# Optimization experiments

Hardware: AMD Instinct MI355X
Metric: run time of the kernel (lower is better)

Reference implementation:

```python
import jax, jax.numpy as jnp
import numpy as np

B, T, H, L, O = 128, 1024, 512, 2, 1
SCALE = 0.02  # keep tanh/sigmoid in sane range


def setup_inputs() -> dict:
    key = jax.random.key(0)
    ks = jax.random.split(key, 13)
    return {
        "input": jax.random.normal(ks[0], (B, 8), jnp.float32),
        "hidden": jax.random.normal(ks[1], (L, B, H), jnp.float32) * 0.5,
        "encoder_outputs": jax.random.normal(ks[2], (B, T, H), jnp.float32),
        "attn_w": jax.random.normal(ks[3], (1, (L + 1) * H), jnp.float32) * SCALE,
        "attn_b": jnp.zeros((1,), jnp.float32),
        "comb_w": jax.random.normal(ks[4], (H, H + O), jnp.float32) * SCALE,
        "comb_b": jnp.zeros((H,), jnp.float32),
        "gru_w_ih": jax.random.normal(ks[5], (L, 3 * H, H), jnp.float32) * SCALE,
        "gru_w_hh": jax.random.normal(ks[6], (L, 3 * H, H), jnp.float32) * SCALE,
        "gru_b_ih": jnp.zeros((L, 3 * H), jnp.float32),
        "gru_b_hh": jnp.zeros((L, 3 * H), jnp.float32),
        "out_w": jax.random.normal(ks[7], (O, H), jnp.float32) * SCALE,
        "out_b": jnp.zeros((O,), jnp.float32),
    }


def reference(input, hidden, encoder_outputs, attn_w, attn_b, comb_w, comb_b,
              gru_w_ih, gru_w_hh, gru_b_ih, gru_b_hh, out_w, out_b):
    # input0 = input[:, -1].unsqueeze(1) -> [B, 1]
    input0 = input[:, -1:]
    # hidden [L,B,H] -> hidden_attn [B, L*H]
    hidden_attn = jnp.transpose(hidden, (1, 0, 2)).reshape(hidden.shape[1], -1)
    # Vectorized additive-attention scores (original loops over T):
    # score[b,t] = [hidden_attn_b ; enc_bt] @ attn_w.T + attn_b
    w = attn_w[0]                      # [(L+1)*H]
    w_h, w_e = w[: L * H], w[L * H:]   # [L*H], [H]
    score = (hidden_attn @ w_h)[:, None] + jnp.einsum('bth,h->bt', encoder_outputs, w_e) + attn_b[0]
    attn_weights = jax.nn.softmax(score, axis=1)          # [B, T]
    attn_applied = jnp.einsum('bt,bth->bh', attn_weights, encoder_outputs)  # [B, H]
    # attn_combine + relu (dropout_p = 0 -> identity)
    comb_in = jnp.concatenate([input0, attn_applied], axis=1)  # [B, 1+H]
    x = jax.nn.relu(comb_in @ comb_w.T + comb_b)               # [B, H]
    # single-step multi-layer GRU (PyTorch gate order: r, z, n)
    new_hidden = []
    for l in range(L):
        gx = x @ gru_w_ih[l].T + gru_b_ih[l]             # [B, 3H]
        gh = hidden[l] @ gru_w_hh[l].T + gru_b_hh[l]     # [B, 3H]
        xr, xz, xn = jnp.split(gx, 3, axis=1)
        hr, hz, hn = jnp.split(gh, 3, axis=1)
        r = jax.nn.sigmoid(xr + hr)
        z = jax.nn.sigmoid(xz + hz)
        n = jnp.tanh(xn + r * hn)
        h_new = (1.0 - z) * n + z * hidden[l]
        new_hidden.append(h_new)
        x = h_new
    hidden_out = jnp.stack(new_hidden, axis=0)           # [L, B, H]
    output = x @ out_w.T + out_b                         # [B, O]
    return output, hidden_out, attn_weights[:, None, :]
```

## Files before the change

### kernel.cpp

```cpp
#include <hip/hip_runtime.h>
#include <math.h>

#define B 128
#define T 1024
#define H 512
#define L 2
#define G3H 1536
#define C 8
#define TC 128
#define TT 8
#define NT (TC / TT)
#define KS 2

#define GLOBAL_AS __attribute__((address_space(1)))
#define LDS_AS    __attribute__((address_space(3)))

typedef __attribute__((ext_vector_type(8))) short bf16x8;
typedef __attribute__((ext_vector_type(4))) float f32x4;

__global__ __launch_bounds__(256, 4)
void attn_fused_kernel(const float* __restrict__ enc,
                       const float* __restrict__ attn_w,
                       float* __restrict__ score_out,
                       float* __restrict__ part,
                       float* __restrict__ stats) {
    int c = blockIdx.x, b = blockIdx.y;
    int tid = threadIdx.x, lane = tid & 63, wave = tid >> 6;
    __shared__ float tile[2][TT * H];
    __shared__ float s_tile[TT];

    const float4 we0 = *(const float4*)(attn_w + L * H + lane * 8);
    const float4 we1 = *(const float4*)(attn_w + L * H + lane * 8 + 4);

    const float* encb = enc + ((size_t)b * T + c * TC) * H;
    const GLOBAL_AS float* gsrc = (const GLOBAL_AS float*)encb;
    LDS_AS float* ldst = (LDS_AS float*)(&tile[0][0]);

#define STAGE(buf, t0)                                                        \
    {                                                                         \
        const GLOBAL_AS float* g = gsrc + (size_t)(t0) * H;                   \
        LDS_AS float* lb = ldst + (buf) * (TT * H);                           \
        _Pragma("unroll")                                                     \
        for (int k = 0; k < 4; k++) {                                         \
            __builtin_amdgcn_global_load_lds(                                 \
                (const GLOBAL_AS void*)(g + k * 1024 + tid * 4),              \
                (LDS_AS void*)(lb + k * 1024 + tid * 4), 16, 0, 0);           \
        }                                                                     \
    }

    float m_run = -1e30f, l_run = 0.0f;
    float accx = 0.0f, accy = 0.0f;

    STAGE(0, 0);
    for (int t = 0; t < NT; t++) {
        __syncthreads();
        if (t + 1 < NT) STAGE((t + 1) & 1, (t + 1) * TT);
        const float* tb = &tile[t & 1][0];

#pragma unroll
        for (int r = 0; r < 2; r++) {
            int row = wave * 2 + r;
            const float* tr = tb + row * H + lane * 8;
            float4 e0 = *(const float4*)(tr);
            float4 e1 = *(const float4*)(tr + 4);
            float d = e0.x * we0.x + e0.y * we0.y + e0.z * we0.z + e0.w * we0.w
                    + e1.x * we1.x + e1.y * we1.y + e1.z * we1.z + e1.w * we1.w;
#pragma unroll
            for (int off = 32; off; off >>= 1) d += __shfl_xor(d, off);
            if (lane == 0) {
                s_tile[row] = d;
                score_out[b * T + c * TC + t * TT + row] = d;
            }
        }
        __builtin_amdgcn_s_waitcnt(0xC07F);
        __builtin_amdgcn_s_barrier();

        float sarr[TT], tmax = -1e30f;
#pragma unroll
        for (int i = 0; i < TT; i++) {
            sarr[i] = s_tile[i];
            tmax = fmaxf(tmax, sarr[i]);
        }
        float m_new = fmaxf(m_run, tmax);
        float alpha = __expf(m_run - m_new);
        accx *= alpha; accy *= alpha;
        float wsum = 0.0f;
#pragma unroll
        for (int i = 0; i < TT; i++) {
            float w = __expf(sarr[i] - m_new);
            wsum += w;
            accx += w * tb[i * H + tid];
            accy += w * tb[i * H + tid + 256];
        }
        l_run = l_run * alpha + wsum;
        m_run = m_new;
    }
    part[((size_t)c * B + b) * H + tid]       = accx;
    part[((size_t)c * B + b) * H + tid + 256] = accy;
    if (tid == 0) {
        stats[(c * B + b) * 2]     = m_run;
        stats[(c * B + b) * 2 + 1] = l_run;
    }
#undef STAGE
}

__global__ void comb_kernel(const float* __restrict__ part,
                            const float* __restrict__ stats,
                            const float* __restrict__ score,
                            const float* __restrict__ input,
                            const float* __restrict__ comb_w,
                            const float* __restrict__ comb_b,
                            float* __restrict__ x_out,
                            float* __restrict__ attnw) {
    int q = blockIdx.x, b = blockIdx.y, tid = threadIdx.x;
    int lane = tid & 63, wave = tid >> 6;
    __shared__ float at[H];

    float mc[C], lc[C], m_fin = -1e30f;
#pragma unroll
    for (int k = 0; k < C; k++) {
        mc[k] = stats[(k * B + b) * 2];
        lc[k] = stats[(k * B + b) * 2 + 1];
        m_fin = fmaxf(m_fin, mc[k]);
    }
    float l_fin = 0.0f;
#pragma unroll
    for (int k = 0; k < C; k++) l_fin += lc[k] * __expf(mc[k] - m_fin);
    float inv = 1.0f / l_fin;
    float ax = 0.0f, ay = 0.0f;
#pragma unroll
    for (int k = 0; k < C; k++) {
        float sc = __expf(mc[k] - m_fin);
        ax += sc * part[((size_t)k * B + b) * H + tid];
        ay += sc * part[((size_t)k * B + b) * H + tid + 256];
    }
    at[tid]       = ax * inv;
    at[tid + 256] = ay * inv;
    if (q == 0) {
        float4 sv = *(const float4*)(score + b * T + tid * 4);
        float4 ov = { __expf(sv.x - m_fin) * inv, __expf(sv.y - m_fin) * inv,
                      __expf(sv.z - m_fin) * inv, __expf(sv.w - m_fin) * inv };
        *(float4*)(attnw + b * T + tid * 4) = ov;
    }
    __syncthreads();

    float in0 = input[b * 8 + 7];
    float areg[8];
#pragma unroll
    for (int j = 0; j < 8; j++) areg[j] = at[j * 64 + lane];
    for (int r = 0; r < 32; r++) {
        int h = q * 128 + wave * 32 + r;
        const float* wr = comb_w + (size_t)h * (H + 1);
        float d = 0.0f;
#pragma unroll
        for (int j = 0; j < 8; j++) d += areg[j] * wr[1 + j * 64 + lane];
#pragma unroll
        for (int off = 32; off; off >>= 1) d += __shfl_xor(d, off);
        if (lane == 0)
            x_out[(size_t)b * H + h] = fmaxf(0.0f, d + in0 * wr[0] + comb_b[h]);
    }
}

__device__ inline short f2bf(float f) {
    union { float f; unsigned u; } v; v.f = f;
    unsigned r = v.u + 0x7fffu + ((v.u >> 16) & 1u);
    return (short)(r >> 16);
}

__device__ inline bf16x8 load_frag(const float* __restrict__ p) {
    float4 a = *(const float4*)p;
    float4 b = *(const float4*)(p + 4);
    bf16x8 r;
    r[0] = f2bf(a.x); r[1] = f2bf(a.y); r[2] = f2bf(a.z); r[3] = f2bf(a.w);
    r[4] = f2bf(b.x); r[5] = f2bf(b.y); r[6] = f2bf(b.z); r[7] = f2bf(b.w);
    return r;
}

__global__ __launch_bounds__(64)
void gemm_mfma_kernel(const float* __restrict__ A0,
                      const float* __restrict__ A1,
                      const float* __restrict__ W0,
                      const float* __restrict__ W1,
                      float* __restrict__ C0,
                      float* __restrict__ C1) {
    int job = blockIdx.x;
    int sel = job & 1, ks = (job >> 1) & (KS - 1), mh = (job >> 2) & 1, nt = job >> 3;
    const float* A = sel ? A1 : A0;
    const float* W = sel ? W1 : W0;
    float* Cp = (sel ? C1 : C0) + (size_t)ks * B * G3H;
    int lane = threadIdx.x;
    int row16 = lane & 15, quad = lane >> 4;
    int n0 = nt * 16, m0 = mh * 64;
    int kb = ks * (H / KS);
    const float* Wp = W + (size_t)(n0 + row16) * H + kb + quad * 8;
    const float* Ap = A + (size_t)(m0 + row16) * H + kb + quad * 8;
    f32x4 acc0 = {0.f, 0.f, 0.f, 0.f}, acc1 = acc0, acc2 = acc0, acc3 = acc0;
#pragma unroll 2
    for (int k = 0; k < H / KS; k += 32) {
        bf16x8 bw = load_frag(Wp + k);
        bf16x8 a0 = load_frag(Ap + k);
        bf16x8 a1 = load_frag(Ap + 16 * H + k);
        bf16x8 a2 = load_frag(Ap + 32 * H + k);
        bf16x8 a3 = load_frag(Ap + 48 * H + k);
        acc0 = __builtin_amdgcn_mfma_f32_16x16x32_bf16(a0, bw, acc0, 0, 0, 0);
        acc1 = __builtin_amdgcn_mfma_f32_16x16x32_bf16(a1, bw, acc1, 0, 0, 0);
        acc2 = __builtin_amdgcn_mfma_f32_16x16x32_bf16(a2, bw, acc2, 0, 0, 0);
        acc3 = __builtin_amdgcn_mfma_f32_16x16x32_bf16(a3, bw, acc3, 0, 0, 0);
    }
    int col = n0 + row16;
    int rb = m0 + quad * 4;
#pragma unroll
    for (int reg = 0; reg < 4; reg++) {
        Cp[(size_t)(rb + reg) * G3H + col]      = acc0[reg];
        Cp[(size_t)(rb + 16 + reg) * G3H + col] = acc1[reg];
        Cp[(size_t)(rb + 32 + reg) * G3H + col] = acc2[reg];
        Cp[(size_t)(rb + 48 + reg) * G3H + col] = acc3[reg];
    }
}

__global__ __launch_bounds__(512)
void gates_kernel(const float* __restrict__ gx,
                  const float* __restrict__ gh,
                  const float* __restrict__ b_ih,
                  const float* __restrict__ b_hh,
                  const float* __restrict__ hprev,
                  float* __restrict__ hid_out,
                  float* __restrict__ x_out,
                  const float* __restrict__ out_w,
                  const float* __restrict__ out_b,
                  float* __restrict__ out,
                  int last) {
    int b = blockIdx.x, h = threadIdx.x;
    int lane = h & 63, wave = h >> 6;
    size_t gb = (size_t)b * G3H;
    float xr = b_ih[h], xz = b_ih[H + h], xn = b_ih[2 * H + h];
    float hr = b_hh[h], hz = b_hh[H + h], hn = b_hh[2 * H + h];
#pragma unroll
    for (int k = 0; k < KS; k++) {
        size_t o = (size_t)k * B * G3H + gb;
        xr += gx[o + h];         xz += gx[o + H + h];     xn += gx[o + 2 * H + h];
        hr += gh[o + h];         hz += gh[o + H + h];     hn += gh[o + 2 * H + h];
    }
    float hp = hprev[(size_t)b * H + h];
    float r = 1.0f / (1.0f + expf(-(xr + hr)));
    float z = 1.0f / (1.0f + expf(-(xz + hz)));
    float n = tanhf(xn + r * hn);
    float hnew = (1.0f - z) * n + z * hp;
    hid_out[(size_t)b * H + h] = hnew;
    x_out[(size_t)b * H + h] = hnew;
    if (last) {
        __shared__ float red[8];
        float d = hnew * out_w[h];
#pragma unroll
        for (int off = 32; off; off >>= 1) d += __shfl_xor(d, off);
        if (lane == 0) red[wave] = d;
        __syncthreads();
        if (h == 0) {
            float s = out_b[0];
#pragma unroll
            for (int i = 0; i < 8; i++) s += red[i];
            out[b] = s;
        }
    }
}

extern "C" void kernel_launch(void* const* d_in, const int* in_sizes, int n_in,
                              void* d_out, int out_size, void* d_ws, size_t ws_size,
                              hipStream_t stream) {
    const float* input  = (const float*)d_in[0];
    const float* hidden = (const float*)d_in[1];
    const float* enc    = (const float*)d_in[2];
    const float* attn_w = (const float*)d_in[3];
    const float* comb_w = (const float*)d_in[5];
    const float* comb_b = (const float*)d_in[6];
    const float* w_ih   = (const float*)d_in[7];
    const float* w_hh   = (const float*)d_in[8];
    const float* b_ih   = (const float*)d_in[9];
    const float* b_hh   = (const float*)d_in[10];
    const float* out_w  = (const float*)d_in[11];
    const float* out_b  = (const float*)d_in[12];

    float* out = (float*)d_out;
    float* hid_out = out + B;
    float* attnw   = out + B + L * B * H;

    float* ws      = (float*)d_ws;
    float* score   = ws;
    float* part    = score + B * T;
    float* stats   = part + C * B * H;
    float* x       = stats + C * B * 2;
    float* gx      = x + B * H;
    float* gh      = gx + KS * B * G3H;

    attn_fused_kernel<<<dim3(C, B), 256, 0, stream>>>(enc, attn_w, score, part, stats);
    comb_kernel<<<dim3(4, B), 256, 0, stream>>>(part, stats, score, input,
                                                comb_w, comb_b, x, attnw);

    for (int l = 0; l < L; l++) {
        const float* hl = hidden + (size_t)l * B * H;
        gemm_mfma_kernel<<<dim3((G3H / 16) * 2 * KS * 2), 64, 0, stream>>>(
            x, hl,
            w_ih + (size_t)l * G3H * H, w_hh + (size_t)l * G3H * H,
            gx, gh);
        gates_kernel<<<dim3(B), 512, 0, stream>>>(
            gx, gh, b_ih + l * G3H, b_hh + l * G3H, hl,
            hid_out + (size_t)l * B * H, x,
            out_w, out_b, out, l == L - 1);
    }
}
```

Measured before the change: 443.7 us.

## Fuse combine, GRU GEMMs and gates into one persistent kernel with grid barriers

Replaces the comb kernel and the per-layer GEMM/gates launches with a single persistent 256-block tail kernel. The stages are separated by a software grid barrier built on an atomic counter and generation word, which the attention kernel resets. This removes four kernel launch gaps. In exchange, the GEMM now runs on only 1024 waves in 256 blocks, and correctness depends on all 256 blocks being co-resident.

```diff
diff --git a/kernel.cpp b/kernel.cpp
--- a/kernel.cpp
+++ b/kernel.cpp
@@ -11,6 +11,8 @@
 #define TT 8
 #define NT (TC / TT)
 #define KS 2
+#define NBLK 256
+#define NJOB ((G3H / 16) * 2 * KS * 2)
 
 #define GLOBAL_AS __attribute__((address_space(1)))
 #define LDS_AS    __attribute__((address_space(3)))
@@ -23,9 +25,12 @@
                        const float* __restrict__ attn_w,
                        float* __restrict__ score_out,
                        float* __restrict__ part,
-                       float* __restrict__ stats) {
+                       float* __restrict__ stats,
+                       unsigned* __restrict__ bar) {
     int c = blockIdx.x, b = blockIdx.y;
     int tid = threadIdx.x, lane = tid & 63, wave = tid >> 6;
+    if (c == 0 && b == 0 && tid == 0)
+        __hip_atomic_store(&bar[0], 0u, __ATOMIC_RELAXED, __HIP_MEMORY_SCOPE_AGENT);
     __shared__ float tile[2][TT * H];
     __shared__ float s_tile[TT];
 
@@ -104,17 +109,50 @@
 #undef STAGE
 }
 
-__global__ void comb_kernel(const float* __restrict__ part,
-                            const float* __restrict__ stats,
-                            const float* __restrict__ score,
-                            const float* __restrict__ input,
-                            const float* __restrict__ comb_w,
-                            const float* __restrict__ comb_b,
-                            float* __restrict__ x_out,
-                            float* __restrict__ attnw) {
-    int q = blockIdx.x, b = blockIdx.y, tid = threadIdx.x;
-    int lane = tid & 63, wave = tid >> 6;
-    __shared__ float at[H];
+__device__ __forceinline__ void grid_barrier(unsigned* bar) {
+    __threadfence();
+    __syncthreads();
+    if (threadIdx.x == 0) {
+        unsigned g = __hip_atomic_load(&bar[1], __ATOMIC_RELAXED,
+                                       __HIP_MEMORY_SCOPE_AGENT);
+        unsigned v = __hip_atomic_fetch_add(&bar[0], 1u, __ATOMIC_ACQ_REL,
+                                            __HIP_MEMORY_SCOPE_AGENT);
+        if (v == NBLK - 1) {
+            __hip_atomic_store(&bar[0], 0u, __ATOMIC_RELAXED,
+                               __HIP_MEMORY_SCOPE_AGENT);
+            __hip_atomic_fetch_add(&bar[1], 1u, __ATOMIC_ACQ_REL,
+                                   __HIP_MEMORY_SCOPE_AGENT);
+        } else {
+            while (__hip_atomic_load(&bar[1], __ATOMIC_ACQUIRE,
+                                     __HIP_MEMORY_SCOPE_AGENT) == g)
+                __builtin_amdgcn_s_sleep(2);
+        }
+    }
+    __syncthreads();
+    __threadfence();
+}
+
+__device__ inline short f2bf(float f) {
+    union { float f; unsigned u; } v; v.f = f;
+    unsigned r = v.u + 0x7fffu + ((v.u >> 16) & 1u);
+    return (short)(r >> 16);
+}
+
+__device__ inline bf16x8 load_frag(const float* p) {
+    float4 a = *(const float4*)p;
+    float4 b = *(const float4*)(p + 4);
+    bf16x8 r;
+    r[0] = f2bf(a.x); r[1] = f2bf(a.y); r[2] = f2bf(a.z); r[3] = f2bf(a.w);
+    r[4] = f2bf(b.x); r[5] = f2bf(b.y); r[6] = f2bf(b.z); r[7] = f2bf(b.w);
+    return r;
+}
+
+__device__ __forceinline__ void comb_item(
+        int item, const float* part, const float* stats, const float* score,
+        const float* input, const float* comb_w, const float* comb_b,
+        float* x_out, float* attnw, float* at) {
+    int q = item >> 7, b = item & (B - 1);
+    int tid = threadIdx.x, lane = tid & 63, wave = tid >> 6;
 
     float mc[C], lc[C], m_fin = -1e30f;
 #pragma unroll
@@ -161,34 +199,14 @@
     }
 }
 
-__device__ inline short f2bf(float f) {
-    union { float f; unsigned u; } v; v.f = f;
-    unsigned r = v.u + 0x7fffu + ((v.u >> 16) & 1u);
-    return (short)(r >> 16);
-}
-
-__device__ inline bf16x8 load_frag(const float* __restrict__ p) {
-    float4 a = *(const float4*)p;
-    float4 b = *(const float4*)(p + 4);
-    bf16x8 r;
-    r[0] = f2bf(a.x); r[1] = f2bf(a.y); r[2] = f2bf(a.z); r[3] = f2bf(a.w);
-    r[4] = f2bf(b.x); r[5] = f2bf(b.y); r[6] = f2bf(b.z); r[7] = f2bf(b.w);
-    return r;
-}
-
-__global__ __launch_bounds__(64)
-void gemm_mfma_kernel(const float* __restrict__ A0,
-                      const float* __restrict__ A1,
-                      const float* __restrict__ W0,
-                      const float* __restrict__ W1,
-                      float* __restrict__ C0,
-                      float* __restrict__ C1) {
-    int job = blockIdx.x;
+__device__ __forceinline__ void gemm_job(
+        int job, const float* A0, const float* A1,
+        const float* W0, const float* W1, float* C0, float* C1) {
     int sel = job & 1, ks = (job >> 1) & (KS - 1), mh = (job >> 2) & 1, nt = job >> 3;
     const float* A = sel ? A1 : A0;
     const float* W = sel ? W1 : W0;
     float* Cp = (sel ? C1 : C0) + (size_t)ks * B * G3H;
-    int lane = threadIdx.x;
+    int lane = threadIdx.x & 63;
     int row16 = lane & 15, quad = lane >> 4;
     int n0 = nt * 16, m0 = mh * 64;
     int kb = ks * (H / KS);
@@ -218,20 +236,9 @@
     }
 }
 
-__global__ __launch_bounds__(512)
-void gates_kernel(const float* __restrict__ gx,
-                  const float* __restrict__ gh,
-                  const float* __restrict__ b_ih,
-                  const float* __restrict__ b_hh,
-                  const float* __restrict__ hprev,
-                  float* __restrict__ hid_out,
-                  float* __restrict__ x_out,
-                  const float* __restrict__ out_w,
-                  const float* __restrict__ out_b,
-                  float* __restrict__ out,
-                  int last) {
-    int b = blockIdx.x, h = threadIdx.x;
-    int lane = h & 63, wave = h >> 6;
+__device__ __forceinline__ float gru_one(
+        int b, int h, const float* gx, const float* gh,
+        const float* b_ih, const float* b_hh, const float* hprev) {
     size_t gb = (size_t)b * G3H;
     float xr = b_ih[h], xz = b_ih[H + h], xn = b_ih[2 * H + h];
     float hr = b_hh[h], hz = b_hh[H + h], hn = b_hh[2 * H + h];
@@ -245,21 +252,51 @@
     float r = 1.0f / (1.0f + expf(-(xr + hr)));
     float z = 1.0f / (1.0f + expf(-(xz + hz)));
     float n = tanhf(xn + r * hn);
-    float hnew = (1.0f - z) * n + z * hp;
-    hid_out[(size_t)b * H + h] = hnew;
-    x_out[(size_t)b * H + h] = hnew;
-    if (last) {
-        __shared__ float red[8];
-        float d = hnew * out_w[h];
-#pragma unroll
-        for (int off = 32; off; off >>= 1) d += __shfl_xor(d, off);
-        if (lane == 0) red[wave] = d;
-        __syncthreads();
-        if (h == 0) {
-            float s = out_b[0];
-#pragma unroll
-            for (int i = 0; i < 8; i++) s += red[i];
-            out[b] = s;
+    return (1.0f - z) * n + z * hp;
+}
+
+__global__ void tail_kernel(const float* input, const float* hidden,
+                            const float* comb_w, const float* comb_b,
+                            const float* w_ih, const float* w_hh,
+                            const float* b_ih, const float* b_hh,
+                            const float* out_w, const float* out_b,
+                            float* out, float* hid_out, float* attnw,
+                            const float* score, const float* part,
+                            const float* stats,
+                            float* x, float* gx, float* gh, unsigned* bar) {
+    __shared__ float at[H];
+    __shared__ float red[4];
+    int tid = threadIdx.x;
+    int wglob = blockIdx.x * 4 + (tid >> 6);
+
+    comb_item(blockIdx.x, part, stats, score, input, comb_w, comb_b, x, attnw, at);
+    __syncthreads();
+    comb_item(blockIdx.x + NBLK, part, stats, score, input, comb_w, comb_b, x, attnw, at);
+
+    for (int l = 0; l < L; l++) {
+        const float* hl = hidden + (size_t)l * B * H;
+        grid_barrier(bar);
+        if (wglob < NJOB)
+            gemm_job(wglob, x, hl,
+                     w_ih + (size_t)l * G3H * H, w_hh + (size_t)l * G3H * H,
+                     gx, gh);
+        grid_barrier(bar);
+        if (blockIdx.x < B) {
+            int b = blockIdx.x;
+            float hn0 = gru_one(b, tid,       gx, gh, b_ih + l * G3H, b_hh + l * G3H, hl);
+            float hn1 = gru_one(b, tid + 256, gx, gh, b_ih + l * G3H, b_hh + l * G3H, hl);
+            float* ho = hid_out + (size_t)l * B * H + (size_t)b * H;
+            ho[tid]       = hn0;  ho[tid + 256]       = hn1;
+            x[(size_t)b * H + tid] = hn0;  x[(size_t)b * H + tid + 256] = hn1;
+            if (l == L - 1) {
+                float d = hn0 * out_w[tid] + hn1 * out_w[tid + 256];
+#pragma unroll
+                for (int off = 32; off; off >>= 1) d += __shfl_xor(d, off);
+                if ((tid & 63) == 0) red[tid >> 6] = d;
+                __syncthreads();
+                if (tid == 0)
+                    out[b] = out_b[0] + red[0] + red[1] + red[2] + red[3];
+            }
         }
     }
 }
@@ -291,20 +328,12 @@
     float* x       = stats + C * B * 2;
     float* gx      = x + B * H;
     float* gh      = gx + KS * B * G3H;
-
-    attn_fused_kernel<<<dim3(C, B), 256, 0, stream>>>(enc, attn_w, score, part, stats);
-    comb_kernel<<<dim3(4, B), 256, 0, stream>>>(part, stats, score, input,
-                                                comb_w, comb_b, x, attnw);
-
-    for (int l = 0; l < L; l++) {
-        const float* hl = hidden + (size_t)l * B * H;
-        gemm_mfma_kernel<<<dim3((G3H / 16) * 2 * KS * 2), 64, 0, stream>>>(
-            x, hl,
-            w_ih + (size_t)l * G3H * H, w_hh + (size_t)l * G3H * H,
-            gx, gh);
-        gates_kernel<<<dim3(B), 512, 0, stream>>>(
-            gx, gh, b_ih + l * G3H, b_hh + l * G3H, hl,
-            hid_out + (size_t)l * B * H, x,
-            out_w, out_b, out, l == L - 1);
-    }
-}
+    unsigned* bar  = (unsigned*)(gh + KS * B * G3H);
+
+    attn_fused_kernel<<<dim3(C, B), 256, 0, stream>>>(enc, attn_w, score, part,
+                                                      stats, bar);
+    tail_kernel<<<dim3(NBLK), 256, 0, stream>>>(
+        input, hidden, comb_w, comb_b, w_ih, w_hh, b_ih, b_hh,
+        out_w, out_b, out, hid_out, attnw, score, part, stats,
+        x, gx, gh, bar);
+}
```

Measured after the change: 772.5 us. +74.1%, slower.

## Deepen encoder-tile prefetch to four smaller buffers with explicit vmcnt waits

Applied to the files above, without the earlier changes.

Shrinks each staged encoder tile from 8 to 4 rows and uses a 4-deep ring of LDS buffers, keeping three tiles of async global-to-LDS loads in flight. Per-iteration waits use explicit vmcnt counts instead of a full syncthreads, and sched barriers stop the compiler from reordering around them. The aim is to hide global memory latency better. The cost is twice as many loop iterations and barriers, plus fragile hand-coded waitcnt encodings.

```diff
diff --git a/kernel.cpp b/kernel.cpp
--- a/kernel.cpp
+++ b/kernel.cpp
@@ -8,8 +8,9 @@
 #define G3H 1536
 #define C 8
 #define TC 128
-#define TT 8
+#define TT 4
 #define NT (TC / TT)
+#define NBUF 4
 #define KS 2
 
 #define GLOBAL_AS __attribute__((address_space(1)))
@@ -26,7 +27,7 @@
                        float* __restrict__ stats) {
     int c = blockIdx.x, b = blockIdx.y;
     int tid = threadIdx.x, lane = tid & 63, wave = tid >> 6;
-    __shared__ float tile[2][TT * H];
+    __shared__ float tile[NBUF][TT * H];
     __shared__ float s_tile[TT];
 
     const float4 we0 = *(const float4*)(attn_w + L * H + lane * 8);
@@ -36,12 +37,12 @@
     const GLOBAL_AS float* gsrc = (const GLOBAL_AS float*)encb;
     LDS_AS float* ldst = (LDS_AS float*)(&tile[0][0]);
 
-#define STAGE(buf, t0)                                                        \
+#define STAGE(t0)                                                             \
     {                                                                         \
-        const GLOBAL_AS float* g = gsrc + (size_t)(t0) * H;                   \
-        LDS_AS float* lb = ldst + (buf) * (TT * H);                           \
+        const GLOBAL_AS float* g = gsrc + (size_t)(t0) * (TT * H);            \
+        LDS_AS float* lb = ldst + ((t0) & (NBUF - 1)) * (TT * H);             \
         _Pragma("unroll")                                                     \
-        for (int k = 0; k < 4; k++) {                                         \
+        for (int k = 0; k < 2; k++) {                                         \
             __builtin_amdgcn_global_load_lds(                                 \
                 (const GLOBAL_AS void*)(g + k * 1024 + tid * 4),              \
                 (LDS_AS void*)(lb + k * 1024 + tid * 4), 16, 0, 0);           \
@@ -51,16 +52,21 @@
     float m_run = -1e30f, l_run = 0.0f;
     float accx = 0.0f, accy = 0.0f;
 
-    STAGE(0, 0);
+    STAGE(0); STAGE(1); STAGE(2);
+
     for (int t = 0; t < NT; t++) {
-        __syncthreads();
-        if (t + 1 < NT) STAGE((t + 1) & 1, (t + 1) * TT);
-        const float* tb = &tile[t & 1][0];
-
-#pragma unroll
-        for (int r = 0; r < 2; r++) {
-            int row = wave * 2 + r;
-            const float* tr = tb + row * H + lane * 8;
+        int rem = NT - 1 - t;
+        if (rem >= 2)      __builtin_amdgcn_s_waitcnt(0x0F74);
+        else if (rem == 1) __builtin_amdgcn_s_waitcnt(0x0F72);
+        else               __builtin_amdgcn_s_waitcnt(0x0F70);
+        __builtin_amdgcn_s_barrier();
+        __builtin_amdgcn_sched_barrier(0);
+        if (t + (NBUF - 1) < NT) STAGE(t + (NBUF - 1));
+
+        const float* tb = &tile[t & (NBUF - 1)][0];
+
+        {
+            const float* tr = tb + wave * H + lane * 8;
             float4 e0 = *(const float4*)(tr);
             float4 e1 = *(const float4*)(tr + 4);
             float d = e0.x * we0.x + e0.y * we0.y + e0.z * we0.z + e0.w * we0.w
@@ -68,12 +74,13 @@
 #pragma unroll
             for (int off = 32; off; off >>= 1) d += __shfl_xor(d, off);
             if (lane == 0) {
-                s_tile[row] = d;
-                score_out[b * T + c * TC + t * TT + row] = d;
+                s_tile[wave] = d;
+                score_out[b * T + c * TC + t * TT + wave] = d;
             }
         }
         __builtin_amdgcn_s_waitcnt(0xC07F);
         __builtin_amdgcn_s_barrier();
+        __builtin_amdgcn_sched_barrier(0);
 
         float sarr[TT], tmax = -1e30f;
 #pragma unroll
```

New measurement: 444.6 us. Within noise of the previous version (+0.2%).
